# Optimization experiments

Measured on AMD Instinct MI355X. Metric: run time of the kernel, lower is better.

## Reference

```python
import jax, jax.numpy as jnp
import numpy as np

RADIUS = 4
SIGMA_1 = 5.0
SIGMA_2 = 1.0


def _gaussian_kernel(dtype):
    # norm.pdf(d)/norm.pdf(0) == exp(-d^2/2)
    x2 = jnp.linspace(-RADIUS, RADIUS, 2 * RADIUS + 1) ** 2
    dist = jnp.sqrt(x2[:, None] + x2[None, :]) / SIGMA_1
    return jnp.exp(-0.5 * dist ** 2).astype(dtype)  # [k, k]


def setup_inputs() -> dict:
    key = jax.random.key(0)
    k1, k2 = jax.random.split(key)
    labels = jax.random.uniform(k1, (16, 20, 256, 256), dtype=jnp.float32)
    inputs = jax.random.uniform(k2, (16, 3, 256, 256), dtype=jnp.float32)
    return {"labels": labels, "inputs": inputs}


def reference(labels, inputs):
    B, K, H, W = labels.shape
    kernel = _gaussian_kernel(labels.dtype)

    # per-class mean color: mean(inputs * probs, HW) / (mean(probs, HW) + 1e-5)
    pmean = jnp.mean(labels, axis=(2, 3))                           # [B, K]
    xmean = jnp.einsum('bchw,bkhw->bkc', inputs, labels) / (H * W)  # [B, K, C]
    class_mean = xmean / (pmean[..., None] + 1e-5)                  # [B, K, C]

    # diff = sum_c (x_c - m_c)^2, expanded to avoid a [B,K,C,H,W] intermediate
    x2sum = jnp.sum(inputs ** 2, axis=1)                            # [B, H, W]
    cross = jnp.einsum('bchw,bkc->bkhw', inputs, class_mean)        # [B, K, H, W]
    m2 = jnp.sum(class_mean ** 2, axis=-1)                          # [B, K]
    diff = x2sum[:, None] - 2.0 * cross + m2[:, :, None, None]      # [B, K, H, W]
    weights = jnp.exp(-(diff ** 2) / (SIGMA_2 ** 2))                # [B, K, H, W]

    def blur(x):  # single-channel gaussian conv, vectorized over B*K
        lhs = x.reshape(B * K, 1, H, W)
        rhs = kernel[None, None]  # [1, 1, k, k]
        y = jax.lax.conv_general_dilated(
            lhs, rhs, window_strides=(1, 1),
            padding=[(RADIUS, RADIUS), (RADIUS, RADIUS)],
            dimension_numbers=('NCHW', 'OIHW', 'NCHW'))
        return y.reshape(B, K, H, W)

    num = jnp.sum(labels * blur(labels * weights), axis=(0, 2, 3))  # [K]
    den = jnp.sum(labels * blur(weights), axis=(0, 2, 3))           # [K]
    loss = jnp.sum(jnp.abs(num / (den + 1e-6)))
    return jnp.asarray(K, labels.dtype) - loss
```

## Files before the change

kernel.cpp:

```cpp
#include <hip/hip_runtime.h>

#define B_ 16
#define K_ 20
#define H_ 256
#define W_ 256
#define HW_ (H_*W_)
#define BK_ (B_*K_)
#define TH_ 64
#define KT_ 5
#define SCH_ 16
#define NBLK_FUSED_ (4*K_*B_)

#define WS_ND_   (SCH_*4*BK_)
#define WS_CNT_  (WS_ND_ + 2*NBLK_FUSED_)

#define G1T 0.980198673f
#define G2T 0.923116346f
#define G3T 0.835270211f
#define G4T 0.726149037f

__device__ __forceinline__ float rfl(float v) {
    return __int_as_float(__builtin_amdgcn_readfirstlane(__float_as_int(v)));
}

__global__ __launch_bounds__(256) void stats_k(const float* __restrict__ labels,
                                               const float* __restrict__ inputs,
                                               float* __restrict__ ws) {
    const int x = threadIdx.x;
    const int chunk = blockIdx.x;
    const int kt = blockIdx.y;
    const int b  = blockIdx.z;
    const int k0 = kt * KT_;
    if (chunk == 0 && kt == 0 && b == 0 && x == 0)
        ((unsigned*)(ws + WS_CNT_))[0] = 0u;

    const int cbase = chunk * (16 * W_ / 4);
    const float4* in0 = (const float4*)inputs + (size_t)b * 3 * (HW_/4) + cbase;
    const float4* in1 = in0 + (HW_/4);
    const float4* in2 = in1 + (HW_/4);
    const float4* lb  = (const float4*)labels + (size_t)(b * K_ + k0) * (HW_/4) + cbase;

    float acc[KT_][4];
#pragma unroll
    for (int kk = 0; kk < KT_; ++kk)
        acc[kk][0] = acc[kk][1] = acc[kk][2] = acc[kk][3] = 0.f;

#pragma unroll
    for (int it = 0; it < 4; ++it) {
        const int idx = it * 256 + x;
        const float4 a0 = in0[idx];
        const float4 a1 = in1[idx];
        const float4 a2 = in2[idx];
        float4 lv[KT_];
#pragma unroll
        for (int kk = 0; kk < KT_; ++kk) lv[kk] = lb[kk * (HW_/4) + idx];
#pragma unroll
        for (int kk = 0; kk < KT_; ++kk) {
            const float4 l = lv[kk];
            acc[kk][0] += (l.x + l.y) + (l.z + l.w);
            acc[kk][1] += fmaf(l.w, a0.w, fmaf(l.z, a0.z, fmaf(l.y, a0.y, l.x * a0.x)));
            acc[kk][2] += fmaf(l.w, a1.w, fmaf(l.z, a1.z, fmaf(l.y, a1.y, l.x * a1.x)));
            acc[kk][3] += fmaf(l.w, a2.w, fmaf(l.z, a2.z, fmaf(l.y, a2.y, l.x * a2.x)));
        }
    }

#pragma unroll
    for (int kk = 0; kk < KT_; ++kk)
#pragma unroll
        for (int q = 0; q < 4; ++q)
            for (int o = 32; o > 0; o >>= 1)
                acc[kk][q] += __shfl_down(acc[kk][q], o);

    __shared__ float sred[4][KT_][4];
    const int widx = x >> 6, lane = x & 63;
    if (lane == 0)
#pragma unroll
        for (int kk = 0; kk < KT_; ++kk)
#pragma unroll
            for (int q = 0; q < 4; ++q) sred[widx][kk][q] = acc[kk][q];
    __syncthreads();
    if (x < KT_ * 4) {
        const int kk = x >> 2, q = x & 3;
        const float v = sred[0][kk][q] + sred[1][kk][q] + sred[2][kk][q] + sred[3][kk][q];
        ws[(chunk * 4 + q) * BK_ + b * K_ + k0 + kk] = v;
    }
}

__global__ __launch_bounds__(256) void fused_k(const float* __restrict__ labels,
                                               const float* __restrict__ inputs,
                                               float* __restrict__ ws,
                                               float* __restrict__ out) {
    const int x = threadIdx.x;
    const int bid = blockIdx.x;
    const int swz = (bid & 7) * (NBLK_FUSED_ / 8) + (bid >> 3);
    const int b   = swz / (4 * K_);
    const int rem = swz - b * (4 * K_);
    const int k   = rem >> 2;
    const int sg  = rem & 3;
    const int bk  = b * K_ + k;
    const int r0  = sg * TH_;

    float s0 = 0.f, s1 = 0.f, s2 = 0.f, s3 = 0.f;
#pragma unroll
    for (int c = 0; c < SCH_; ++c) {
        const float* p = ws + c * 4 * BK_;
        s0 += p[bk]; s1 += p[BK_ + bk]; s2 += p[2*BK_ + bk]; s3 += p[3*BK_ + bk];
    }
    const float dnv = s0 + 1e-5f * (float)HW_;
    const float c0 = s1 / dnv, c1 = s2 / dnv, c2 = s3 / dnv;
    const float tc0 = rfl(2.f * c0), tc1 = rfl(2.f * c1), tc2 = rfl(2.f * c2);
    const float m2v = rfl(c0*c0 + c1*c1 + c2*c2);

    const float* lb  = labels + (size_t)bk * HW_;
    const float* i0p = inputs + (size_t)b * 3 * HW_;
    const float* i1p = i0p + HW_;
    const float* i2p = i1p + HW_;

    __shared__ float sv[2][W_ + 8];
    if (x < 4) {
        sv[0][x] = 0.f; sv[0][W_ + 4 + x] = 0.f;
        sv[1][x] = 0.f; sv[1][W_ + 4 + x] = 0.f;
    }

    float rl[8];
#pragma unroll
    for (int i = 0; i < 8; ++i) {
        const int gr = r0 - 4 + i;
        rl[i] = (gr >= 0) ? lb[gr * W_ + x] : 0.f;
    }
    float hl  = lb[(r0 + 4) * W_ + x];
    float hi0 = i0p[r0 * W_ + x];
    float hi1 = i1p[r0 * W_ + x];
    float hi2 = i2p[r0 * W_ + x];

    __syncthreads();

    float num = 0.f, den = 0.f;
#pragma unroll 1
    for (int ro = 0; ro < TH_ / 8; ++ro) {
#pragma unroll
        for (int u = 0; u < 8; ++u) {
            const int orow = r0 + ro * 8 + u;
            float nl = 0.f;
            if (orow + 5 < H_) nl = lb[(orow + 5) * W_ + x];
            const int nir = (orow + 1 < H_) ? orow + 1 : H_ - 1;
            const float ni0 = i0p[nir * W_ + x];
            const float ni1 = i1p[nir * W_ + x];
            const float ni2 = i2p[nir * W_ + x];
            const float vbl = fmaf(G4T, rl[u] + hl,
                              fmaf(G3T, rl[(u+1)&7] + rl[(u+7)&7],
                              fmaf(G2T, rl[(u+2)&7] + rl[(u+6)&7],
                              fmaf(G1T, rl[(u+3)&7] + rl[(u+5)&7], rl[(u+4)&7]))));
            const int bf = u & 1;
            sv[bf][4 + x] = vbl;
            __syncthreads();
            const float* s = &sv[bf][x];
            const float bl = fmaf(G4T, s[0] + s[8],
                             fmaf(G3T, s[1] + s[7],
                             fmaf(G2T, s[2] + s[6],
                             fmaf(G1T, s[3] + s[5], s[4]))));
            const float d = fmaf(hi0, hi0 - tc0,
                            fmaf(hi1, hi1 - tc1,
                            fmaf(hi2, hi2 - tc2, m2v)));
            const float w = __expf(-d * d);
            const float t = w * bl;
            den += t;
            num = fmaf(rl[(u + 4) & 7], t, num);
            rl[u] = hl;
            hl = nl; hi0 = ni0; hi1 = ni1; hi2 = ni2;
        }
    }

    const int widx = x >> 6, lane = x & 63;
    for (int o = 32; o > 0; o >>= 1) { num += __shfl_down(num, o); den += __shfl_down(den, o); }
    __shared__ float rb[4][2];
    __shared__ unsigned sdone;
    __syncthreads();
    if (lane == 0) { rb[widx][0] = num; rb[widx][1] = den; }
    __syncthreads();
    if (x == 0) {
        const float fn = rb[0][0] + rb[1][0] + rb[2][0] + rb[3][0];
        const float fd = rb[0][1] + rb[1][1] + rb[2][1] + rb[3][1];
        float2* nd2 = (float2*)(ws + WS_ND_);
        nd2[k * 64 + b * 4 + sg] = make_float2(fn, fd);
        __threadfence();
        sdone = atomicAdd((unsigned*)(ws + WS_CNT_), 1u);
    }
    __syncthreads();
    if (sdone == (unsigned)(NBLK_FUSED_ - 1)) {
        __threadfence();
        if (x < 64) {
            float term = 0.f;
            if (x < K_) {
                const float2* nd2 = (const float2*)(ws + WS_ND_);
                float ns = 0.f, ds = 0.f;
                for (int i = 0; i < 64; ++i) {
                    const float2 v = nd2[x * 64 + i];
                    ns += v.x; ds += v.y;
                }
                term = fabsf(ns / (ds + 1e-6f));
            }
            for (int o = 32; o > 0; o >>= 1) term += __shfl_down(term, o);
            if (x == 0) out[0] = (float)K_ - term;
        }
    }
}

extern "C" void kernel_launch(void* const* d_in, const int* in_sizes, int n_in,
                              void* d_out, int out_size, void* d_ws, size_t ws_size,
                              hipStream_t stream) {
    const float* labels = (const float*)d_in[0];
    const float* inputs = (const float*)d_in[1];
    float* ws = (float*)d_ws;

    stats_k<<<dim3(SCH_, K_ / KT_, B_), 256, 0, stream>>>(labels, inputs, ws);
    fused_k<<<NBLK_FUSED_, 256, 0, stream>>>(labels, inputs, ws, (float*)d_out);
}
```

Before: 197.6 us.

## Batch eight rows per barrier with register prefetch of next row block

The fused blur/weight loop now computes vertical blur for eight output rows at once into a double-buffered shared array of eight rows. This needs one __syncthreads per eight rows instead of one per row. Labels and input channels for the next batch are loaded into registers ahead of use, and the weights are computed one batch in advance. The cost is higher register and LDS use per block, which may lower occupancy.

```diff
diff --git a/kernel.cpp b/kernel.cpp
--- a/kernel.cpp
+++ b/kernel.cpp
@@ -7,6 +7,7 @@
 #define HW_ (H_*W_)
 #define BK_ (B_*K_)
 #define TH_ 64
+#define BATCH_ 8
 #define KT_ 5
 #define SCH_ 16
 #define NBLK_FUSED_ (4*K_*B_)
@@ -85,6 +86,8 @@
         ws[(chunk * 4 + q) * BK_ + b * K_ + k0 + kk] = v;
     }
 }
+
+#define CAT(m) (((m) < 8) ? ring[(m)&7] : PL[(m)&7])
 
 __global__ __launch_bounds__(256) void fused_k(const float* __restrict__ labels,
                                                const float* __restrict__ inputs,
@@ -116,58 +119,75 @@
     const float* i1p = i0p + HW_;
     const float* i2p = i1p + HW_;
 
-    __shared__ float sv[2][W_ + 8];
-    if (x < 4) {
-        sv[0][x] = 0.f; sv[0][W_ + 4 + x] = 0.f;
-        sv[1][x] = 0.f; sv[1][W_ + 4 + x] = 0.f;
-    }
-
-    float rl[8];
+    __shared__ float sv[2][BATCH_][W_ + 8];
+    if (x < 128) {
+        const int bu = x >> 6, j = (x >> 3) & 7, p = x & 7;
+        const int col = (p < 4) ? p : (W_ + p);
+        sv[bu][j][col] = 0.f;
+    }
+
+    float ring[8], PL[8], PW[8];
 #pragma unroll
     for (int i = 0; i < 8; ++i) {
         const int gr = r0 - 4 + i;
-        rl[i] = (gr >= 0) ? lb[gr * W_ + x] : 0.f;
-    }
-    float hl  = lb[(r0 + 4) * W_ + x];
-    float hi0 = i0p[r0 * W_ + x];
-    float hi1 = i1p[r0 * W_ + x];
-    float hi2 = i2p[r0 * W_ + x];
-
+        ring[i] = (gr >= 0) ? lb[gr * W_ + x] : 0.f;
+    }
+#pragma unroll
+    for (int i = 0; i < 8; ++i)
+        PL[i] = lb[(r0 + 4 + i) * W_ + x];
+#pragma unroll
+    for (int i = 0; i < 8; ++i) {
+        const int r = r0 + i;
+        const float a0 = i0p[r * W_ + x], a1 = i1p[r * W_ + x], a2 = i2p[r * W_ + x];
+        const float d = fmaf(a0, a0 - tc0, fmaf(a1, a1 - tc1, fmaf(a2, a2 - tc2, m2v)));
+        PW[i] = __expf(-d * d);
+    }
     __syncthreads();
 
     float num = 0.f, den = 0.f;
 #pragma unroll 1
-    for (int ro = 0; ro < TH_ / 8; ++ro) {
-#pragma unroll
-        for (int u = 0; u < 8; ++u) {
-            const int orow = r0 + ro * 8 + u;
-            float nl = 0.f;
-            if (orow + 5 < H_) nl = lb[(orow + 5) * W_ + x];
-            const int nir = (orow + 1 < H_) ? orow + 1 : H_ - 1;
-            const float ni0 = i0p[nir * W_ + x];
-            const float ni1 = i1p[nir * W_ + x];
-            const float ni2 = i2p[nir * W_ + x];
-            const float vbl = fmaf(G4T, rl[u] + hl,
-                              fmaf(G3T, rl[(u+1)&7] + rl[(u+7)&7],
-                              fmaf(G2T, rl[(u+2)&7] + rl[(u+6)&7],
-                              fmaf(G1T, rl[(u+3)&7] + rl[(u+5)&7], rl[(u+4)&7]))));
-            const int bf = u & 1;
-            sv[bf][4 + x] = vbl;
-            __syncthreads();
-            const float* s = &sv[bf][x];
+    for (int bt = 0; bt < TH_ / BATCH_; ++bt) {
+        const int R = r0 + bt * BATCH_;
+        const int bf = bt & 1;
+        float NL[8];
+#pragma unroll
+        for (int i = 0; i < 8; ++i) {
+            const int gr = R + 12 + i;
+            NL[i] = (gr < H_) ? lb[gr * W_ + x] : 0.f;
+        }
+        float a0v[8], a1v[8], a2v[8];
+#pragma unroll
+        for (int i = 0; i < 8; ++i) {
+            int r = R + 8 + i; r = (r < H_) ? r : H_ - 1;
+            a0v[i] = i0p[r * W_ + x]; a1v[i] = i1p[r * W_ + x]; a2v[i] = i2p[r * W_ + x];
+        }
+#pragma unroll
+        for (int j = 0; j < 8; ++j) {
+            const float v = fmaf(G4T, CAT(j) + CAT(j+8),
+                            fmaf(G3T, CAT(j+1) + CAT(j+7),
+                            fmaf(G2T, CAT(j+2) + CAT(j+6),
+                            fmaf(G1T, CAT(j+3) + CAT(j+5), CAT(j+4)))));
+            sv[bf][j][4 + x] = v;
+        }
+        __syncthreads();
+#pragma unroll
+        for (int j = 0; j < 8; ++j) {
+            const float* s = &sv[bf][j][x];
             const float bl = fmaf(G4T, s[0] + s[8],
                              fmaf(G3T, s[1] + s[7],
                              fmaf(G2T, s[2] + s[6],
                              fmaf(G1T, s[3] + s[5], s[4]))));
-            const float d = fmaf(hi0, hi0 - tc0,
-                            fmaf(hi1, hi1 - tc1,
-                            fmaf(hi2, hi2 - tc2, m2v)));
+            const float t = PW[j] * bl;
+            den += t;
+            num = fmaf(CAT(j+4), t, num);
+        }
+#pragma unroll
+        for (int i = 0; i < 8; ++i) {
+            const float d = fmaf(a0v[i], a0v[i] - tc0,
+                            fmaf(a1v[i], a1v[i] - tc1,
+                            fmaf(a2v[i], a2v[i] - tc2, m2v)));
             const float w = __expf(-d * d);
-            const float t = w * bl;
-            den += t;
-            num = fmaf(rl[(u + 4) & 7], t, num);
-            rl[u] = hl;
-            hl = nl; hi0 = ni0; hi1 = ni1; hi2 = ni2;
+            ring[i] = PL[i]; PL[i] = NL[i]; PW[i] = w;
         }
     }
 
```

New measurement: 197.2 us. About the same (-0.2%).
